# Performance work log

Measured on AMD Instinct MI355X. Metric: run time of the kernel, lower is better.

Reference implementation:

```python
import jax, jax.numpy as jnp
import numpy as np

TH_DEPTH3 = [-0.67, 0.0, 0.67]


def packbits_big(bits):
    """Pack 0/1 values along the last axis into uint8, big-endian bit order.

    Equivalent to the torch packbits: pad last dim to a multiple of 8 with
    zeros, group into bytes, weight by [128,64,...,1], sum as uint8.
    """
    n = bits.shape[-1]
    pad = (-n) % 8
    if pad:
        pad_widths = [(0, 0)] * (bits.ndim - 1) + [(0, pad)]
        bits = jnp.pad(bits, pad_widths)
    grouped = bits.reshape(bits.shape[:-1] + (-1, 8))  # [..., n/8, 8]
    weights = (1 << jnp.arange(7, -1, -1)).astype(jnp.uint8)  # big-endian
    return (grouped.astype(jnp.uint8) * weights).sum(axis=-1, dtype=jnp.uint8)


def setup_inputs() -> dict:
    key = jax.random.key(0)
    k1, _ = jax.random.split(key)
    B, N = 2048, 32768
    x = jax.random.normal(k1, (B, N), dtype=jnp.float32)
    depth_ths = jnp.asarray(TH_DEPTH3, dtype=jnp.float32)  # [d] = [3]
    return {"x": x, "depth_ths": depth_ths}


def reference(x, depth_ths):
    # x: [b, n] -> compare against each threshold: [b, d, n] booleans
    bits = (x[:, None, :] > depth_ths[None, :, None])
    # bit-pack along last axis -> uint8 [b, d, ceil(n/8)]
    return packbits_big(bits)
```

## Files before the change

### kernel.cpp

```cpp
#include <hip/hip_runtime.h>


constexpr int B_ROWS = 2048;
constexpr int N_COLS = 32768;
constexpr int NB = N_COLS / 8;
constexpr int D = 3;
constexpr int GP = 4;
constexpr int GROUPS = NB / GP;

typedef float vfloat4 __attribute__((ext_vector_type(4)));
typedef int   vint4   __attribute__((ext_vector_type(4)));

__device__ __forceinline__ unsigned pack8(const vfloat4& a, const vfloat4& b, float t) {
    unsigned p = 0;
    p = (p << 1) | (a.x > t ? 1u : 0u);
    p = (p << 1) | (a.y > t ? 1u : 0u);
    p = (p << 1) | (a.z > t ? 1u : 0u);
    p = (p << 1) | (a.w > t ? 1u : 0u);
    p = (p << 1) | (b.x > t ? 1u : 0u);
    p = (p << 1) | (b.y > t ? 1u : 0u);
    p = (p << 1) | (b.z > t ? 1u : 0u);
    p = (p << 1) | (b.w > t ? 1u : 0u);
    return p;
}

__global__ __launch_bounds__(256) void Binarize_52913997086767_kernel(
    const float* __restrict__ x,
    const float* __restrict__ ths,
    int* __restrict__ out)
{
    unsigned idx = blockIdx.x * 256u + threadIdx.x;
    unsigned row = idx >> 10;
    unsigned grp = (idx & 1023u) << 2;

    const vfloat4* xp = reinterpret_cast<const vfloat4*>(
        x + ((size_t)row << 15) + ((size_t)grp << 3));

    vfloat4 v[8];
#pragma unroll
    for (int i = 0; i < 8; ++i)
        v[i] = __builtin_nontemporal_load(&xp[i]);

    float t0 = ths[0];
    float t1 = ths[1];
    float t2 = ths[2];

    vint4 w0, w1, w2;
    w0.x = (int)pack8(v[0], v[1], t0);
    w0.y = (int)pack8(v[2], v[3], t0);
    w0.z = (int)pack8(v[4], v[5], t0);
    w0.w = (int)pack8(v[6], v[7], t0);

    w1.x = (int)pack8(v[0], v[1], t1);
    w1.y = (int)pack8(v[2], v[3], t1);
    w1.z = (int)pack8(v[4], v[5], t1);
    w1.w = (int)pack8(v[6], v[7], t1);

    w2.x = (int)pack8(v[0], v[1], t2);
    w2.y = (int)pack8(v[2], v[3], t2);
    w2.z = (int)pack8(v[4], v[5], t2);
    w2.w = (int)pack8(v[6], v[7], t2);

    int* obase = out + (size_t)row * (D * NB) + grp;
    __builtin_nontemporal_store(w0, reinterpret_cast<vint4*>(obase));
    __builtin_nontemporal_store(w1, reinterpret_cast<vint4*>(obase + NB));
    __builtin_nontemporal_store(w2, reinterpret_cast<vint4*>(obase + 2 * NB));
}

extern "C" void kernel_launch(void* const* d_in, const int* in_sizes, int n_in,
                              void* d_out, int out_size, void* d_ws, size_t ws_size,
                              hipStream_t stream) {
    const float* x   = (const float*)d_in[0];
    const float* ths = (const float*)d_in[1];
    int* out = (int*)d_out;

    const int total_threads = B_ROWS * GROUPS;
    dim3 grid(total_threads / 256);
    dim3 block(256);
    Binarize_52913997086767_kernel<<<grid, block, 0, stream>>>(x, ths, out);
}
```

Measured before the change: 433.6 us.

## Use grid-strided per-thread byte groups with coalesced scalar stores

Each thread now handles one 8-float group per iteration, four iterations strided across the whole grid, instead of four adjacent groups. All loads are issued before any compute to raise memory-level parallelism. Output becomes one 32-bit store per threshold instead of a 128-bit store. Loads switch from nontemporal to regular. Adjacent threads now touch adjacent 32-byte input chunks, trading wider per-thread vectors for better coalescing across the wavefront.

Measured after the change: 395.4 us. 1.1x faster.

```diff
diff --git a/kernel.cpp b/kernel.cpp
--- a/kernel.cpp
+++ b/kernel.cpp
@@ -5,11 +5,11 @@
 constexpr int N_COLS = 32768;
 constexpr int NB = N_COLS / 8;
 constexpr int D = 3;
-constexpr int GP = 4;
-constexpr int GROUPS = NB / GP;
+constexpr int ITERS = 4;
+constexpr int BLOCKS = (B_ROWS * NB) / (256 * ITERS);
+constexpr unsigned STRIDE = BLOCKS * 256u;
 
 typedef float vfloat4 __attribute__((ext_vector_type(4)));
-typedef int   vint4   __attribute__((ext_vector_type(4)));
 
 __device__ __forceinline__ unsigned pack8(const vfloat4& a, const vfloat4& b, float t) {
     unsigned p = 0;
@@ -29,42 +29,39 @@
     const float* __restrict__ ths,
     int* __restrict__ out)
 {
-    unsigned idx = blockIdx.x * 256u + threadIdx.x;
-    unsigned row = idx >> 10;
-    unsigned grp = (idx & 1023u) << 2;
-
-    const vfloat4* xp = reinterpret_cast<const vfloat4*>(
-        x + ((size_t)row << 15) + ((size_t)grp << 3));
-
-    vfloat4 v[8];
-#pragma unroll
-    for (int i = 0; i < 8; ++i)
-        v[i] = __builtin_nontemporal_load(&xp[i]);
+    unsigned tid0 = blockIdx.x * 256u + threadIdx.x;
 
     float t0 = ths[0];
     float t1 = ths[1];
     float t2 = ths[2];
 
-    vint4 w0, w1, w2;
-    w0.x = (int)pack8(v[0], v[1], t0);
-    w0.y = (int)pack8(v[2], v[3], t0);
-    w0.z = (int)pack8(v[4], v[5], t0);
-    w0.w = (int)pack8(v[6], v[7], t0);
+    vfloat4 a[ITERS], b[ITERS];
+#pragma unroll
+    for (int i = 0; i < ITERS; ++i) {
+        unsigned idx  = tid0 + (unsigned)i * STRIDE;
+        unsigned row  = idx >> 12;
+        unsigned grp  = idx & 4095u;
+        const vfloat4* xp = reinterpret_cast<const vfloat4*>(
+            x + ((size_t)row << 15) + ((size_t)grp << 3));
+        a[i] = xp[0];
+        b[i] = xp[1];
+    }
 
-    w1.x = (int)pack8(v[0], v[1], t1);
-    w1.y = (int)pack8(v[2], v[3], t1);
-    w1.z = (int)pack8(v[4], v[5], t1);
-    w1.w = (int)pack8(v[6], v[7], t1);
+#pragma unroll
+    for (int i = 0; i < ITERS; ++i) {
+        unsigned idx  = tid0 + (unsigned)i * STRIDE;
+        unsigned row  = idx >> 12;
+        unsigned grp  = idx & 4095u;
 
-    w2.x = (int)pack8(v[0], v[1], t2);
-    w2.y = (int)pack8(v[2], v[3], t2);
-    w2.z = (int)pack8(v[4], v[5], t2);
-    w2.w = (int)pack8(v[6], v[7], t2);
+        unsigned p0 = pack8(a[i], b[i], t0);
+        unsigned p1 = pack8(a[i], b[i], t1);
+        unsigned p2 = pack8(a[i], b[i], t2);
 
-    int* obase = out + (size_t)row * (D * NB) + grp;
-    __builtin_nontemporal_store(w0, reinterpret_cast<vint4*>(obase));
-    __builtin_nontemporal_store(w1, reinterpret_cast<vint4*>(obase + NB));
-    __builtin_nontemporal_store(w2, reinterpret_cast<vint4*>(obase + 2 * NB));
+        int* o = out + (size_t)row * (D * NB) + grp;
+        __builtin_nontemporal_store((int)p0, o);
+        __builtin_nontemporal_store((int)p1, o + NB);
+        __builtin_nontemporal_store((int)p2, o + 2 * NB);
+    }
 }
 
 extern "C" void kernel_launch(void* const* d_in, const int* in_sizes, int n_in,
@@ -74,8 +71,7 @@
     const float* ths = (const float*)d_in[1];
     int* out = (int*)d_out;
 
-    const int total_threads = B_ROWS * GROUPS;
-    dim3 grid(total_threads / 256);
+    dim3 grid(BLOCKS);
     dim3 block(256);
     Binarize_52913997086767_kernel<<<grid, block, 0, stream>>>(x, ths, out);
 }
```
